# Optimization experiments

Measured on AMD Instinct MI355X. Metric: run time of the kernel, lower is better.

Reference implementation:

```python
import jax, jax.numpy as jnp
import numpy as np

KERNEL_SIZE = 3  # matches init kwarg

def setup_inputs() -> dict:
    key = jax.random.key(0)
    k1, k2, k3, k4 = jax.random.split(key, 4)
    N, C, L, OUT = 32, 64, 2048, 128
    inp = jax.random.normal(k1, (N, C, L), dtype=jnp.float32)
    # adjacency-like dense matrix (tree adjacency may be sparse; dense here)
    m = jax.random.uniform(k2, (N, L, L), dtype=jnp.float32)
    W = jax.random.normal(k3, (OUT, KERNEL_SIZE * C), dtype=jnp.float32) * 0.05
    b = jax.random.normal(k4, (OUT,), dtype=jnp.float32)
    return {"input": inp, "m": m, "W": W, "b": b}

def reference(input, m, W, b):
    # propagate features over the tree adjacency kernel_size-1 times
    ys = [input]
    y = input
    for _ in range(KERNEL_SIZE - 1):
        y = jnp.matmul(y, m)          # (N, C, L) @ (N, L, L) -> (N, C, L)
        ys.append(y)
    cat = jnp.concatenate(ys, axis=1)  # (N, k*C, L)
    # 1x1 conv == channel projection
    out = jnp.einsum('oc,ncl->nol', W, cat) + b[None, :, None]
    return out
```

## Files before the change

kernel.cpp:

```cpp
#include <hip/hip_runtime.h>
#include <hip/hip_bf16.h>

#define NB   32
#define CH   64
#define LL   2048
#define OUTC 128

typedef float  f32x4  __attribute__((ext_vector_type(4)));
typedef short  s16x8  __attribute__((ext_vector_type(8)));
typedef short  s16x4  __attribute__((ext_vector_type(4)));
typedef unsigned short u16;

__device__ __forceinline__ u16 f2bf(float f) {
  unsigned int u = __builtin_bit_cast(unsigned int, f);
  u += 0x7FFFu + ((u >> 16) & 1u);
  return (u16)(u >> 16);
}

__device__ __forceinline__ s16x8 pack8c(const float* v) {
  s16x8 r;
#pragma unroll
  for (int j = 0; j < 8; j += 2) {
    __hip_bfloat162 h = __float22bfloat162_rn(make_float2(v[j], v[j + 1]));
    short2 s;
    __builtin_memcpy(&s, &h, sizeof(s));
    r[j] = s.x; r[j + 1] = s.y;
  }
  return r;
}

__device__ __forceinline__ s16x4 pack4c(const f32x4& v) {
  s16x4 r;
  __hip_bfloat162 h0 = __float22bfloat162_rn(make_float2(v[0], v[1]));
  __hip_bfloat162 h1 = __float22bfloat162_rn(make_float2(v[2], v[3]));
  short2 s0, s1;
  __builtin_memcpy(&s0, &h0, sizeof(s0));
  __builtin_memcpy(&s1, &h1, sizeof(s1));
  r[0] = s0.x; r[1] = s0.y; r[2] = s1.x; r[3] = s1.y;
  return r;
}

#define NX (NB * CH * LL)
#define NW (OUTC * 3 * CH)
__global__ __launch_bounds__(256)
void cvt_inputs(const float* __restrict__ x, const float* __restrict__ W,
                u16* __restrict__ xb, u16* __restrict__ Wb)
{
  const size_t t8 = ((size_t)blockIdx.x * 256 + threadIdx.x) * 8;
  if (t8 < NX) {
    float v[8];
    *(f32x4*)(v)     = *(const f32x4*)(x + t8);
    *(f32x4*)(v + 4) = *(const f32x4*)(x + t8 + 4);
    *(s16x8*)(xb + t8) = pack8c(v);
  } else if (t8 - NX < NW) {
    const size_t w8 = t8 - NX;
    float v[8];
    *(f32x4*)(v)     = *(const f32x4*)(W + w8);
    *(f32x4*)(v + 4) = *(const f32x4*)(W + w8 + 4);
    *(s16x8*)(Wb + w8) = pack8c(v);
  }
}

__global__ __launch_bounds__(256, 3)
void prop1_pack(const u16* __restrict__ xb, const float* __restrict__ m,
                u16* __restrict__ y1, u16* __restrict__ mP)
{
  __shared__ float smem[3][32 * 128];

  const int n    = blockIdx.x >> 4;
  const int lt   = blockIdx.x & 15;
  const int tid  = threadIdx.x;
  const int wave = tid >> 6;
  const int lane = tid & 63;
  const int l15  = lane & 15;
  const int g4   = lane >> 4;
  const int colb = lt * 128 + wave * 32;

  const float* mn   = m + (size_t)n * LL * LL + lt * 128;
  const float* gsrc = mn + (size_t)(wave * 8 + (lane >> 5)) * LL + (lane & 31) * 4;
  const u16*   ap   = xb + (size_t)n * CH * LL + (size_t)l15 * LL + g4 * 8;
  u16* q0 = mP + (((size_t)n * 64 * LL + colb + l15) * 4 + g4) * 8;
  u16* o  = y1 + (size_t)n * CH * LL + colb + l15;

  f32x4 acc[4][2];
#pragma unroll
  for (int f = 0; f < 4; ++f)
#pragma unroll
    for (int h = 0; h < 2; ++h)
#pragma unroll
      for (int r = 0; r < 4; ++r) acc[f][h][r] = 0.f;

  s16x8 aP[4], aQ[4];

#define ALOAD(R, KB)                                                          \
  { const u16* _ap = ap + (KB) * 32;                                          \
    _Pragma("unroll") for (int f = 0; f < 4; ++f)                             \
      R[f] = *(const s16x8*)(_ap + (size_t)(f * 16) * LL); }

#define GLOAD(BI, KB)                                                         \
  { float* _sb = smem[BI];                                                    \
    _Pragma("unroll") for (int i = 0; i < 4; ++i) {                           \
      const float* _g = gsrc + (size_t)((KB) * 32 + i * 2) * LL;              \
      __builtin_amdgcn_global_load_lds(                                       \
        (const __attribute__((address_space(1))) void*)_g,                    \
        (__attribute__((address_space(3))) void*)(_sb + (wave * 4 + i) * 256),\
        16, 0, 0); } }

  ALOAD(aP, 0)
  __builtin_amdgcn_sched_barrier(0);
  GLOAD(0, 0) GLOAD(1, 1)
  __builtin_amdgcn_sched_barrier(0);
  asm volatile("s_waitcnt vmcnt(4)" ::: "memory");
  __builtin_amdgcn_s_barrier();
  __builtin_amdgcn_sched_barrier(0);

#define K1_STEP(KB, CUR, NXT, GI, BI, VN, DOA, DOG, DOBAR)                    \
  {                                                                           \
    if (DOA) {                                                                \
      ALOAD(NXT, (KB) + 1)                                                    \
      __builtin_amdgcn_sched_barrier(0);                                      \
    }                                                                         \
    if (DOG) {                                                                \
      GLOAD(GI, (KB) + 2)                                                     \
      __builtin_amdgcn_sched_barrier(0);                                      \
    }                                                                         \
    const float* _t = smem[BI] + wave * 32 + l15;                             \
    float _bv0[8], _bv1[8];                                                   \
    _Pragma("unroll") for (int j = 0; j < 8; ++j) {                           \
      _bv0[j] = _t[(g4 * 8 + j) * 128];                                       \
      _bv1[j] = _t[(g4 * 8 + j) * 128 + 16];                                  \
    }                                                                         \
    s16x8 _b0 = pack8c(_bv0), _b1 = pack8c(_bv1);                             \
    u16* _q = q0 + (size_t)(KB) * 65536;                                      \
    *(s16x8*)(_q)       = _b0;                                                \
    *(s16x8*)(_q + 512) = _b1;                                                \
    _Pragma("unroll") for (int f = 0; f < 4; ++f) {                           \
      acc[f][0] = __builtin_amdgcn_mfma_f32_16x16x32_bf16(CUR[f], _b0, acc[f][0], 0, 0, 0); \
      acc[f][1] = __builtin_amdgcn_mfma_f32_16x16x32_bf16(CUR[f], _b1, acc[f][1], 0, 0, 0); \
    }                                                                         \
    if (DOBAR) {                                                              \
      __builtin_amdgcn_sched_barrier(0);                                      \
      asm volatile("s_waitcnt vmcnt(" VN ")" ::: "memory");                   \
      __builtin_amdgcn_s_barrier();                                           \
      __builtin_amdgcn_sched_barrier(0);                                      \
    }                                                                         \
  }

  K1_STEP(0, aP, aQ, 2, 0, "10", 1, 1, 1)
#pragma unroll 1
  for (int kb = 1; kb <= 55; kb += 6) {
    K1_STEP(kb,     aQ, aP, 0, 1, "12", 1, 1, 1)
    K1_STEP(kb + 1, aP, aQ, 1, 2, "12", 1, 1, 1)
    K1_STEP(kb + 2, aQ, aP, 2, 0, "12", 1, 1, 1)
    K1_STEP(kb + 3, aP, aQ, 0, 1, "12", 1, 1, 1)
    K1_STEP(kb + 4, aQ, aP, 1, 2, "12", 1, 1, 1)
    K1_STEP(kb + 5, aP, aQ, 2, 0, "12", 1, 1, 1)
  }
  K1_STEP(61, aQ, aP, 0, 1, "12", 1, 1, 1)
  K1_STEP(62, aP, aQ, 0, 2, "8",  1, 0, 1)
  K1_STEP(63, aQ, aP, 0, 0, "0",  0, 0, 0)

#pragma unroll
  for (int f = 0; f < 4; ++f)
#pragma unroll
    for (int r = 0; r < 4; ++r) {
      const int row = f * 16 + g4 * 4 + r;
      o[(size_t)row * LL]      = f2bf(acc[f][0][r]);
      o[(size_t)row * LL + 16] = f2bf(acc[f][1][r]);
    }
}

__global__ __launch_bounds__(256, 3)
void prop2_proj(const u16* __restrict__ y1, const u16* __restrict__ mP,
                const u16* __restrict__ xb, const u16* __restrict__ Wb,
                const float* __restrict__ bias, float* __restrict__ out)
{
  __shared__ u16 yT[128 * 72];

  const int n    = blockIdx.x >> 4;
  const int lt   = blockIdx.x & 15;
  const int tid  = threadIdx.x;
  const int wave = tid >> 6;
  const int lane = tid & 63;
  const int l15  = lane & 15;
  const int g4   = lane >> 4;
  const int colb = lt * 128 + wave * 32;

  const u16* mq = mP + (((size_t)n * 64 * LL + colb + l15) * 4 + g4) * 8;
  const u16* ap = y1 + (size_t)n * CH * LL + (size_t)l15 * LL + g4 * 8;

  f32x4 acc[4][2];
#pragma unroll
  for (int f = 0; f < 4; ++f)
#pragma unroll
    for (int h = 0; h < 2; ++h)
#pragma unroll
      for (int r = 0; r < 4; ++r) acc[f][h][r] = 0.f;

  s16x8 bA0, bA1, bB0, bB1, aA[4], aB[4];

#define K2_LOAD(B0, B1, AV, KB)                                              \
  {                                                                          \
    const u16* _mq = mq + (size_t)(KB) * 65536;                              \
    B0 = *(const s16x8*)(_mq);                                               \
    B1 = *(const s16x8*)(_mq + 512);                                         \
    const u16* _ap = ap + (KB) * 32;                                         \
    _Pragma("unroll") for (int f = 0; f < 4; ++f)                            \
      AV[f] = *(const s16x8*)(_ap + (size_t)(f * 16) * LL);                  \
  }

#define K2_COMP(B0, B1, AV)                                                  \
  _Pragma("unroll") for (int f = 0; f < 4; ++f) {                            \
    acc[f][0] = __builtin_amdgcn_mfma_f32_16x16x32_bf16(AV[f], B0, acc[f][0], 0, 0, 0); \
    acc[f][1] = __builtin_amdgcn_mfma_f32_16x16x32_bf16(AV[f], B1, acc[f][1], 0, 0, 0); \
  }

  K2_LOAD(bA0, bA1, aA, 63)
#pragma unroll 1
  for (int kb = 63; kb >= 1; kb -= 2) {
    K2_LOAD(bB0, bB1, aB, kb - 1)
    K2_COMP(bA0, bA1, aA)
    if (kb - 2 >= 0) K2_LOAD(bA0, bA1, aA, kb - 2)
    K2_COMP(bB0, bB1, aB)
  }

#pragma unroll
  for (int f = 0; f < 4; ++f)
#pragma unroll
    for (int h = 0; h < 2; ++h) {
      const int c = wave * 32 + l15 + 16 * h;
      *(s16x4*)(&yT[c * 72 + f * 16 + g4 * 4]) = pack4c(acc[f][h]);
    }
  __syncthreads();

  f32x4 acc2[8][2];
#pragma unroll
  for (int f = 0; f < 8; ++f)
#pragma unroll
    for (int h = 0; h < 2; ++h)
#pragma unroll
      for (int r = 0; r < 4; ++r) acc2[f][h][r] = 0.f;

  const size_t cb = (size_t)n * CH * LL + colb + l15;
  const u16* xp  = xb + cb + (size_t)(g4 * 8) * LL;
  const u16* y1p = y1 + cb + (size_t)(g4 * 8) * LL;
  const u16* wq  = Wb + (size_t)l15 * 192 + g4 * 8;

#pragma unroll
  for (int kc = 0; kc < 6; ++kc) {
    const int k0 = kc * 32;
    s16x8 b0, b1;
    if (kc < 4) {
      const u16* src = (kc < 2) ? (xp + (size_t)k0 * LL)
                                : (y1p + (size_t)(k0 - 64) * LL);
#pragma unroll
      for (int j = 0; j < 8; ++j) {
        b0[j] = (short)src[(size_t)j * LL];
        b1[j] = (short)src[(size_t)j * LL + 16];
      }
    } else {
      const int rb = (kc - 4) * 32 + g4 * 8;
      b0 = *(const s16x8*)(&yT[(wave * 32 + l15) * 72 + rb]);
      b1 = *(const s16x8*)(&yT[(wave * 32 + l15 + 16) * 72 + rb]);
    }
#pragma unroll
    for (int f = 0; f < 8; ++f) {
      s16x8 af = *(const s16x8*)(wq + (size_t)(f * 16) * 192 + k0);
      acc2[f][0] = __builtin_amdgcn_mfma_f32_16x16x32_bf16(af, b0, acc2[f][0], 0, 0, 0);
      acc2[f][1] = __builtin_amdgcn_mfma_f32_16x16x32_bf16(af, b1, acc2[f][1], 0, 0, 0);
    }
  }

  float* op = out + (size_t)n * OUTC * LL + colb + l15;
#pragma unroll
  for (int f = 0; f < 8; ++f)
#pragma unroll
    for (int r = 0; r < 4; ++r) {
      const int row = f * 16 + g4 * 4 + r;
      op[(size_t)row * LL]      = acc2[f][0][r] + bias[row];
      op[(size_t)row * LL + 16] = acc2[f][1][r] + bias[row];
    }
}

extern "C" void kernel_launch(void* const* d_in, const int* in_sizes, int n_in,
                              void* d_out, int out_size, void* d_ws, size_t ws_size,
                              hipStream_t stream)
{
  const float* x = (const float*)d_in[0];
  const float* m = (const float*)d_in[1];
  const float* W = (const float*)d_in[2];
  const float* b = (const float*)d_in[3];
  float* out = (float*)d_out;

  u16* y1 = (u16*)d_ws;
  u16* xb = y1 + (size_t)NB * CH * LL;
  u16* Wb = xb + (size_t)NB * CH * LL;
  u16* mP = (u16*)((char*)d_ws + (25u << 20));

  cvt_inputs<<<dim3(2060), dim3(256), 0, stream>>>(x, W, xb, Wb);
  prop1_pack<<<dim3(NB * 16), dim3(256), 0, stream>>>(xb, m, y1, mP);
  prop2_proj<<<dim3(NB * 16), dim3(256), 0, stream>>>(y1, mP, xb, Wb, b, out);
}
```

Measured before the change: 271.3 us.

## Widen prop1 column tile to 256 per block, halving grid size

The first propagation kernel now handles 256 columns of m per block instead of 128, so each wave computes 64 columns with a 4x4 accumulator array and each A-fragment load feeds twice as many MFMAs. The LDS staging buffer doubles to 96KB, the m tile load layout is redone to read full 1KB rows per wave, and the wait counts are adjusted for the extra loads in flight. The grid drops to 256 blocks, which is about one block per CU on MI355X, and occupancy falls because of the larger LDS and register footprint. That risks less latency hiding on what is mostly a bandwidth-bound stream over m.

New measurement: 262.5 us. 3.3% less time.

```diff
diff --git a/kernel.cpp b/kernel.cpp
--- a/kernel.cpp
+++ b/kernel.cpp
@@ -61,32 +61,32 @@
   }
 }
 
-__global__ __launch_bounds__(256, 3)
+__global__ __launch_bounds__(256)
 void prop1_pack(const u16* __restrict__ xb, const float* __restrict__ m,
                 u16* __restrict__ y1, u16* __restrict__ mP)
 {
-  __shared__ float smem[3][32 * 128];
-
-  const int n    = blockIdx.x >> 4;
-  const int lt   = blockIdx.x & 15;
+  __shared__ float smem[3][32 * 256];
+
+  const int n    = blockIdx.x >> 3;
+  const int lt   = blockIdx.x & 7;
   const int tid  = threadIdx.x;
   const int wave = tid >> 6;
   const int lane = tid & 63;
   const int l15  = lane & 15;
   const int g4   = lane >> 4;
-  const int colb = lt * 128 + wave * 32;
-
-  const float* mn   = m + (size_t)n * LL * LL + lt * 128;
-  const float* gsrc = mn + (size_t)(wave * 8 + (lane >> 5)) * LL + (lane & 31) * 4;
+  const int colb = lt * 256 + wave * 64;
+
+  const float* mn   = m + (size_t)n * LL * LL + lt * 256;
+  const float* gsrc = mn + (size_t)wave * LL + lane * 4;
   const u16*   ap   = xb + (size_t)n * CH * LL + (size_t)l15 * LL + g4 * 8;
   u16* q0 = mP + (((size_t)n * 64 * LL + colb + l15) * 4 + g4) * 8;
   u16* o  = y1 + (size_t)n * CH * LL + colb + l15;
 
-  f32x4 acc[4][2];
+  f32x4 acc[4][4];
 #pragma unroll
   for (int f = 0; f < 4; ++f)
 #pragma unroll
-    for (int h = 0; h < 2; ++h)
+    for (int h = 0; h < 4; ++h)
 #pragma unroll
       for (int r = 0; r < 4; ++r) acc[f][h][r] = 0.f;
 
@@ -99,18 +99,18 @@
 
 #define GLOAD(BI, KB)                                                         \
   { float* _sb = smem[BI];                                                    \
-    _Pragma("unroll") for (int i = 0; i < 4; ++i) {                           \
-      const float* _g = gsrc + (size_t)((KB) * 32 + i * 2) * LL;              \
+    _Pragma("unroll") for (int i = 0; i < 8; ++i) {                           \
+      const float* _g = gsrc + (size_t)((KB) * 32 + i * 4) * LL;              \
       __builtin_amdgcn_global_load_lds(                                       \
         (const __attribute__((address_space(1))) void*)_g,                    \
-        (__attribute__((address_space(3))) void*)(_sb + (wave * 4 + i) * 256),\
+        (__attribute__((address_space(3))) void*)(_sb + i * 1024 + wave * 256),\
         16, 0, 0); } }
 
   ALOAD(aP, 0)
   __builtin_amdgcn_sched_barrier(0);
   GLOAD(0, 0) GLOAD(1, 1)
   __builtin_amdgcn_sched_barrier(0);
-  asm volatile("s_waitcnt vmcnt(4)" ::: "memory");
+  asm volatile("s_waitcnt vmcnt(8)" ::: "memory");
   __builtin_amdgcn_s_barrier();
   __builtin_amdgcn_sched_barrier(0);
 
@@ -124,20 +124,20 @@
       GLOAD(GI, (KB) + 2)                                                     \
       __builtin_amdgcn_sched_barrier(0);                                      \
     }                                                                         \
-    const float* _t = smem[BI] + wave * 32 + l15;                             \
-    float _bv0[8], _bv1[8];                                                   \
-    _Pragma("unroll") for (int j = 0; j < 8; ++j) {                           \
-      _bv0[j] = _t[(g4 * 8 + j) * 128];                                       \
-      _bv1[j] = _t[(g4 * 8 + j) * 128 + 16];                                  \
+    const float* _t = smem[BI] + wave * 64 + l15;                             \
+    s16x8 _b[4];                                                              \
+    _Pragma("unroll") for (int h = 0; h < 4; ++h) {                           \
+      float _bv[8];                                                           \
+      _Pragma("unroll") for (int j = 0; j < 8; ++j)                           \
+        _bv[j] = _t[(g4 * 8 + j) * 256 + h * 16];                             \
+      _b[h] = pack8c(_bv);                                                    \
     }                                                                         \
-    s16x8 _b0 = pack8c(_bv0), _b1 = pack8c(_bv1);                             \
     u16* _q = q0 + (size_t)(KB) * 65536;                                      \
-    *(s16x8*)(_q)       = _b0;                                                \
-    *(s16x8*)(_q + 512) = _b1;                                                \
-    _Pragma("unroll") for (int f = 0; f < 4; ++f) {                           \
-      acc[f][0] = __builtin_amdgcn_mfma_f32_16x16x32_bf16(CUR[f], _b0, acc[f][0], 0, 0, 0); \
-      acc[f][1] = __builtin_amdgcn_mfma_f32_16x16x32_bf16(CUR[f], _b1, acc[f][1], 0, 0, 0); \
-    }                                                                         \
+    _Pragma("unroll") for (int h = 0; h < 4; ++h)                             \
+      *(s16x8*)(_q + h * 512) = _b[h];                                        \
+    _Pragma("unroll") for (int f = 0; f < 4; ++f)                             \
+      _Pragma("unroll") for (int h = 0; h < 4; ++h)                           \
+        acc[f][h] = __builtin_amdgcn_mfma_f32_16x16x32_bf16(CUR[f], _b[h], acc[f][h], 0, 0, 0); \
     if (DOBAR) {                                                              \
       __builtin_amdgcn_sched_barrier(0);                                      \
       asm volatile("s_waitcnt vmcnt(" VN ")" ::: "memory");                   \
@@ -146,28 +146,29 @@
     }                                                                         \
   }
 
-  K1_STEP(0, aP, aQ, 2, 0, "10", 1, 1, 1)
+  K1_STEP(0, aP, aQ, 2, 0, "16", 1, 1, 1)
 #pragma unroll 1
   for (int kb = 1; kb <= 55; kb += 6) {
-    K1_STEP(kb,     aQ, aP, 0, 1, "12", 1, 1, 1)
-    K1_STEP(kb + 1, aP, aQ, 1, 2, "12", 1, 1, 1)
-    K1_STEP(kb + 2, aQ, aP, 2, 0, "12", 1, 1, 1)
-    K1_STEP(kb + 3, aP, aQ, 0, 1, "12", 1, 1, 1)
-    K1_STEP(kb + 4, aQ, aP, 1, 2, "12", 1, 1, 1)
-    K1_STEP(kb + 5, aP, aQ, 2, 0, "12", 1, 1, 1)
-  }
-  K1_STEP(61, aQ, aP, 0, 1, "12", 1, 1, 1)
-  K1_STEP(62, aP, aQ, 0, 2, "8",  1, 0, 1)
+    K1_STEP(kb,     aQ, aP, 0, 1, "20", 1, 1, 1)
+    K1_STEP(kb + 1, aP, aQ, 1, 2, "20", 1, 1, 1)
+    K1_STEP(kb + 2, aQ, aP, 2, 0, "20", 1, 1, 1)
+    K1_STEP(kb + 3, aP, aQ, 0, 1, "20", 1, 1, 1)
+    K1_STEP(kb + 4, aQ, aP, 1, 2, "20", 1, 1, 1)
+    K1_STEP(kb + 5, aP, aQ, 2, 0, "20", 1, 1, 1)
+  }
+  K1_STEP(61, aQ, aP, 0, 1, "20", 1, 1, 1)
+  K1_STEP(62, aP, aQ, 0, 2, "12", 1, 0, 1)
   K1_STEP(63, aQ, aP, 0, 0, "0",  0, 0, 0)
 
 #pragma unroll
   for (int f = 0; f < 4; ++f)
 #pragma unroll
-    for (int r = 0; r < 4; ++r) {
-      const int row = f * 16 + g4 * 4 + r;
-      o[(size_t)row * LL]      = f2bf(acc[f][0][r]);
-      o[(size_t)row * LL + 16] = f2bf(acc[f][1][r]);
-    }
+    for (int h = 0; h < 4; ++h)
+#pragma unroll
+      for (int r = 0; r < 4; ++r) {
+        const int row = f * 16 + g4 * 4 + r;
+        o[(size_t)row * LL + h * 16] = f2bf(acc[f][h][r]);
+      }
 }
 
 __global__ __launch_bounds__(256, 3)
@@ -298,6 +299,6 @@
   u16* mP = (u16*)((char*)d_ws + (25u << 20));
 
   cvt_inputs<<<dim3(2060), dim3(256), 0, stream>>>(x, W, xb, Wb);
-  prop1_pack<<<dim3(NB * 16), dim3(256), 0, stream>>>(xb, m, y1, mP);
+  prop1_pack<<<dim3(NB * 8), dim3(256), 0, stream>>>(xb, m, y1, mP);
   prop2_proj<<<dim3(NB * 16), dim3(256), 0, stream>>>(y1, mP, xb, Wb, b, out);
 }
```
